# Performance work log

Measured on AMD Instinct MI355X. Metric: run time of the kernel, lower is better.

## Reference

```python
import jax, jax.numpy as jnp
import numpy as np

B, Q, K = 16, 8192, 8192
D_QK, D_V = 64, 64      # raw query/key and value feature dims
H = 8                    # num_heads
DP = 128                 # proj_qks output dim (per default MLP [128, 128])
VP = 64                  # proj_vs output dim (per default MLP [128, 64])
LN_EPS = 1e-6            # flax LayerNorm default


def setup_inputs() -> dict:
    key = jax.random.key(0)
    ks_ = jax.random.split(key, 12)
    f = lambda k, s: jax.random.normal(k, s, jnp.float32)
    return {
        "qs": f(ks_[0], (B, Q, D_QK)),
        "ks": f(ks_[1], (B, K, D_QK)),
        "vs": f(ks_[2], (B, K, D_V)),
        "qs_s": f(ks_[3], (B, Q, D_QK)),
        "ks_s": f(ks_[4], (B, K, D_QK)),
        "valid_lens": jax.random.randint(ks_[5], (B,), 1, K + 1, jnp.int32),
        # proj_qks = MLP([128, 128], gelu): Dense(128) -> gelu -> Dense(128)
        "Wq1": f(ks_[6], (2 * D_QK, DP)) / np.sqrt(2 * D_QK).astype(np.float32),
        "bq1": jnp.zeros((DP,), jnp.float32),
        "Wq2": f(ks_[7], (DP, DP)) / np.sqrt(DP).astype(np.float32),
        "bq2": jnp.zeros((DP,), jnp.float32),
        # proj_vs = MLP([128, 64], gelu): Dense(128) -> gelu -> Dense(64)
        "Wv1": f(ks_[8], (D_V, DP)) / np.sqrt(D_V).astype(np.float32),
        "bv1": jnp.zeros((DP,), jnp.float32),
        "Wv2": f(ks_[9], (DP, VP)) / np.sqrt(DP).astype(np.float32),
        "bv2": jnp.zeros((VP,), jnp.float32),
        "ln_scale": jnp.ones((VP,), jnp.float32),
        "ln_bias": jnp.zeros((VP,), jnp.float32),
    }


def _mlp2(x, W1, b1, W2, b2):
    # Dense -> gelu (tanh approx, flax default) -> Dense
    return jax.nn.gelu(x @ W1 + b1) @ W2 + b2


def reference(qs, ks, vs, qs_s, ks_s, valid_lens,
              Wq1, bq1, Wq2, bq2, Wv1, bv1, Wv2, bv2,
              ln_scale, ln_bias):
    Kl, D = ks.shape[-2], ks.shape[-1]  # D taken BEFORE stacking, as in source
    scale = D ** 0.25
    # stack spatial features then feature-map MLPs
    q = _mlp2(jnp.concatenate([qs_s, qs], axis=-1), Wq1, bq1, Wq2, bq2) / scale
    k = _mlp2(jnp.concatenate([ks_s, ks], axis=-1), Wq1, bq1, Wq2, bq2) / scale
    v = _mlp2(vs, Wv1, bv1, Wv2, bv2)
    # valid-length masking of keys, mean-style normalization of values
    mask = (jnp.arange(Kl)[None, :] < valid_lens[:, None]).astype(k.dtype)[..., None]
    k = k * mask
    v = v / valid_lens[:, None, None].astype(v.dtype)
    Bn, Qn = q.shape[0], q.shape[1]
    q = q.reshape(Bn, Qn, H, DP // H)   # B Q H d
    k = k.reshape(Bn, Kl, H, DP // H)   # B K H d
    v = v.reshape(Bn, Kl, H, VP // H)   # B K H e
    # linear attention: KV outer-product summary then apply queries
    kv = jnp.einsum('bkhd,bkhe->bhde', k, v)          # B H d e
    ctx = jnp.einsum('bqhd,bhde->bqhe', q, kv)        # B Q H e
    ctx = ctx.reshape(Bn, Qn, VP)
    # LayerNorm over last dim
    mu = ctx.mean(-1, keepdims=True)
    var = ((ctx - mu) ** 2).mean(-1, keepdims=True)
    return (ctx - mu) * jax.lax.rsqrt(var + LN_EPS) * ln_scale + ln_bias
```

## Files before the change

### kernel.cpp

```cpp
#include <hip/hip_runtime.h>
#include <hip/hip_bf16.h>


typedef __attribute__((ext_vector_type(8))) short short8;
typedef __attribute__((ext_vector_type(4))) float f32x4;
typedef unsigned int u32;
typedef unsigned short u16;

#define MFMA(A,B,C) __builtin_amdgcn_mfma_f32_16x16x32_bf16((A),(B),(C),0,0,0)
#define SBAR() __builtin_amdgcn_sched_barrier(0)

#define LDH 136
#define LDT 40
#define INVS 0.3535533905932738f

__device__ __forceinline__ u16 bfc(float x){
  __hip_bfloat16 h = __float2bfloat16(x);
  return __bfloat16_as_ushort(h);
}
__device__ __forceinline__ u32 pack2(float a, float b){
  return (u32)bfc(a) | ((u32)bfc(b) << 16);
}
__device__ __forceinline__ float b2f(u16 w){
  return __uint_as_float(((u32)w) << 16);
}
__device__ __forceinline__ short8 cvt8(f32x4 lo, f32x4 hi){
  short8 r;
  r[0]=(short)bfc(lo[0]); r[1]=(short)bfc(lo[1]);
  r[2]=(short)bfc(lo[2]); r[3]=(short)bfc(lo[3]);
  r[4]=(short)bfc(hi[0]); r[5]=(short)bfc(hi[1]);
  r[6]=(short)bfc(hi[2]); r[7]=(short)bfc(hi[3]);
  return r;
}
__device__ __forceinline__ float gelu_f(float x){
  float s = x*x;
  float u = x * __builtin_fmaf(s, 0.035677408136300125f, 0.7978845608028654f);
  float e = __builtin_amdgcn_exp2f(u * -2.885390081777927f);
  return x * __builtin_amdgcn_rcpf(1.0f + e);
}

__global__ void dk_prep(const float* __restrict__ Wq1, const float* __restrict__ Wq2,
                        const float* __restrict__ Wv1, const float* __restrict__ Wv2,
                        u16* __restrict__ wt){
  int i = blockIdx.x*256 + threadIdx.x;
  int e = i & 7;
  int lane = (i >> 3) & 63;
  int chunk = i >> 9;
  int c = lane & 15, g = lane >> 4;
  int k0 = 8*g + e;
  float v;
  if (chunk < 32){
    int mt = chunk >> 2, ks4 = chunk & 3;
    v = Wq1[(ks4*32 + k0)*128 + mt*16 + c];
  } else if (chunk < 64){
    int ch = chunk - 32; int mt = ch >> 2, ks4 = ch & 3;
    v = Wq2[(ks4*32 + k0)*128 + mt*16 + c] * INVS;
  } else if (chunk < 80){
    int ch = chunk - 64; int mt = ch >> 1, ks2 = ch & 1;
    v = Wv1[(ks2*32 + k0)*128 + mt*16 + c];
  } else {
    int ch = chunk - 80; int n2 = ch >> 2, ks4 = ch & 3;
    v = Wv2[(ks4*32 + k0)*64 + n2*16 + c];
  }
  wt[i] = bfc(v);
}

__global__ __launch_bounds__(128, 2) void dk_stage1(
    const float* __restrict__ ksp, const float* __restrict__ kssp,
    const float* __restrict__ vsp, const int* __restrict__ vlen,
    const float* __restrict__ bq1, const float* __restrict__ bq2,
    const float* __restrict__ bv1, const float* __restrict__ bv2,
    const u16* __restrict__ wt, float* __restrict__ kvgr, int repmask)
{
  __shared__ u16 sA[2][5120];
  __shared__ u16 sB[2][2560];
  const int tid = threadIdx.x;
  const int w = tid >> 6, l = tid & 63;
  const int c = l & 15, g = l >> 4;

  int pfx = (l < 16) ? ((vlen[l] + 63) >> 6) : 0;
  #pragma unroll
  for (int m=1; m<16; m<<=1){
    int v = __shfl_up(pfx, m, 64);
    if (l >= m) pfx += v;
  }
  const int T = __shfl(pfx, 15, 64);
  const int t = blockIdx.x;
  if (t >= T) return;
  unsigned long long mk = __ballot(l < 16 && pfx <= t);
  const int b = __popcll(mk);
  const int jb = t - (b ? __shfl(pfx, b-1, 64) : 0);
  const int len = vlen[b];
  const int rbase = jb*64 + w*32;
  if (rbase >= len) return;
  const int rep = t & repmask;
  const size_t row0 = (size_t)b*8192 + rbase;

  u16* H1 = sA[w];
  u16* KT = sA[w];
  u16* VT = sB[w];
  const u16* Wq1t = wt;
  const u16* Wq2t = wt + 16384;
  const u16* Wv1t = wt + 32768;
  const u16* Wv2t = wt + 40960;
  const f32x4 z4 = {0.f,0.f,0.f,0.f};

  {
    f32x4 xvf[8];
    #pragma unroll
    for (int ks2=0; ks2<2; ++ks2){
      #pragma unroll
      for (int nt=0; nt<2; ++nt){
        const float* src = vsp + (row0 + nt*16 + c)*64 + ks2*32 + 8*g;
        xvf[(ks2*2+nt)*2+0] = *(const f32x4*)src;
        xvf[(ks2*2+nt)*2+1] = *(const f32x4*)(src+4);
      }
    }
    SBAR();
    short8 xv[2][2];
    #pragma unroll
    for (int ks2=0; ks2<2; ++ks2)
      #pragma unroll
      for (int nt=0; nt<2; ++nt)
        xv[ks2][nt] = cvt8(xvf[(ks2*2+nt)*2+0], xvf[(ks2*2+nt)*2+1]);
    f32x4 av[8][2];
    #pragma unroll
    for (int mt=0; mt<8; ++mt){ av[mt][0]=z4; av[mt][1]=z4; }
    #pragma unroll
    for (int ks2=0; ks2<2; ++ks2){
      short8 wa[8];
      #pragma unroll
      for (int mt=0; mt<8; ++mt)
        wa[mt] = *(const short8*)&Wv1t[((mt*2+ks2)*64 + l)*8];
      SBAR();
      #pragma unroll
      for (int mt=0; mt<8; ++mt){
        av[mt][0] = MFMA(wa[mt], xv[ks2][0], av[mt][0]);
        av[mt][1] = MFMA(wa[mt], xv[ks2][1], av[mt][1]);
      }
    }
    #pragma unroll
    for (int mt=0; mt<8; ++mt){
      const f32x4 bia = *(const f32x4*)&bv1[mt*16 + 4*g];
      #pragma unroll
      for (int nt=0; nt<2; ++nt){
        uint2 pp;
        pp.x = pack2(gelu_f(av[mt][nt][0]+bia[0]), gelu_f(av[mt][nt][1]+bia[1]));
        pp.y = pack2(gelu_f(av[mt][nt][2]+bia[2]), gelu_f(av[mt][nt][3]+bia[3]));
        *(uint2*)&H1[(nt*16 + c)*LDH + mt*16 + 4*g] = pp;
      }
    }
  }
  {
    f32x4 acv[2][4];
    #pragma unroll
    for (int n2=0; n2<4; ++n2){ acv[0][n2]=z4; acv[1][n2]=z4; }
    #pragma unroll
    for (int ks4=0; ks4<4; ++ks4){
      short8 wb[4];
      #pragma unroll
      for (int n2=0; n2<4; ++n2)
        wb[n2] = *(const short8*)&Wv2t[((n2*4+ks4)*64 + l)*8];
      SBAR();
      const short8 ah0 = *(const short8*)&H1[(c     )*LDH + ks4*32 + 8*g];
      const short8 ah1 = *(const short8*)&H1[(16 + c)*LDH + ks4*32 + 8*g];
      #pragma unroll
      for (int n2=0; n2<4; ++n2){
        acv[0][n2] = MFMA(ah0, wb[n2], acv[0][n2]);
        acv[1][n2] = MFMA(ah1, wb[n2], acv[1][n2]);
      }
    }
    #pragma unroll
    for (int n2=0; n2<4; ++n2){
      const float bb = bv2[n2*16 + c];
      #pragma unroll
      for (int mt=0; mt<2; ++mt){
        uint2 pp;
        pp.x = pack2(acv[mt][n2][0]+bb, acv[mt][n2][1]+bb);
        pp.y = pack2(acv[mt][n2][2]+bb, acv[mt][n2][3]+bb);
        *(uint2*)&VT[(n2*16+c)*LDT + mt*16 + 4*g] = pp;
      }
    }
  }
  {
    f32x4 xkf[16];
    #pragma unroll
    for (int ks4=0; ks4<4; ++ks4){
      #pragma unroll
      for (int nt=0; nt<2; ++nt){
        const int kk = ks4*32 + 8*g;
        const float* src = (ks4 < 2) ? (kssp + (row0 + nt*16 + c)*64 + kk)
                                     : (ksp  + (row0 + nt*16 + c)*64 + (kk - 64));
        xkf[(ks4*2+nt)*2+0] = *(const f32x4*)src;
        xkf[(ks4*2+nt)*2+1] = *(const f32x4*)(src+4);
      }
    }
    SBAR();
    short8 xk[4][2];
    #pragma unroll
    for (int ks4=0; ks4<4; ++ks4)
      #pragma unroll
      for (int nt=0; nt<2; ++nt)
        xk[ks4][nt] = cvt8(xkf[(ks4*2+nt)*2+0], xkf[(ks4*2+nt)*2+1]);
    f32x4 acc[8][2];
    #pragma unroll
    for (int mt=0; mt<8; ++mt){ acc[mt][0]=z4; acc[mt][1]=z4; }
    #pragma unroll
    for (int ks4=0; ks4<4; ++ks4){
      short8 wa[8];
      #pragma unroll
      for (int mt=0; mt<8; ++mt)
        wa[mt] = *(const short8*)&Wq1t[((mt*4+ks4)*64 + l)*8];
      SBAR();
      #pragma unroll
      for (int mt=0; mt<8; ++mt){
        acc[mt][0] = MFMA(wa[mt], xk[ks4][0], acc[mt][0]);
        acc[mt][1] = MFMA(wa[mt], xk[ks4][1], acc[mt][1]);
      }
    }
    #pragma unroll
    for (int mt=0; mt<8; ++mt){
      const f32x4 bia = *(const f32x4*)&bq1[mt*16 + 4*g];
      #pragma unroll
      for (int nt=0; nt<2; ++nt){
        uint2 pp;
        pp.x = pack2(gelu_f(acc[mt][nt][0]+bia[0]), gelu_f(acc[mt][nt][1]+bia[1]));
        pp.y = pack2(gelu_f(acc[mt][nt][2]+bia[2]), gelu_f(acc[mt][nt][3]+bia[3]));
        *(uint2*)&H1[(nt*16 + c)*LDH + mt*16 + 4*g] = pp;
      }
    }
  }
  {
    f32x4 acc2[2][8];
    #pragma unroll
    for (int n2=0; n2<8; ++n2){ acc2[0][n2]=z4; acc2[1][n2]=z4; }
    #pragma unroll
    for (int ks4=0; ks4<4; ++ks4){
      short8 wb[8];
      #pragma unroll
      for (int n2=0; n2<8; ++n2)
        wb[n2] = *(const short8*)&Wq2t[((n2*4+ks4)*64 + l)*8];
      SBAR();
      const short8 ah0 = *(const short8*)&H1[(c     )*LDH + ks4*32 + 8*g];
      const short8 ah1 = *(const short8*)&H1[(16 + c)*LDH + ks4*32 + 8*g];
      #pragma unroll
      for (int n2=0; n2<8; ++n2){
        acc2[0][n2] = MFMA(ah0, wb[n2], acc2[0][n2]);
        acc2[1][n2] = MFMA(ah1, wb[n2], acc2[1][n2]);
      }
    }
    #pragma unroll
    for (int n2=0; n2<8; ++n2){
      const float bb = bq2[n2*16 + c] * INVS;
      #pragma unroll
      for (int mt=0; mt<2; ++mt){
        const int r0 = rbase + mt*16 + 4*g;
        float v0 = (r0+0 < len) ? acc2[mt][n2][0] + bb : 0.f;
        float v1 = (r0+1 < len) ? acc2[mt][n2][1] + bb : 0.f;
        float v2 = (r0+2 < len) ? acc2[mt][n2][2] + bb : 0.f;
        float v3 = (r0+3 < len) ? acc2[mt][n2][3] + bb : 0.f;
        uint2 pp; pp.x = pack2(v0,v1); pp.y = pack2(v2,v3);
        *(uint2*)&KT[(n2*16 + c)*LDT + mt*16 + 4*g] = pp;
      }
    }
  }
  {
    short8 zf = {0,0,0,0,0,0,0,0};
    f32x4 kvacc[8];
    #pragma unroll
    for (int h=0; h<8; ++h) kvacc[h] = z4;
    #pragma unroll
    for (int h=0; h<8; ++h){
      const short8 ka = *(const short8*)&KT[(h*16 + c)*LDT + 8*g];
      short8 vb = zf;
      if (c < 8) vb = *(const short8*)&VT[(h*8 + c)*LDT + 8*g];
      kvacc[h] = MFMA(ka, vb, kvacc[h]);
    }
    if (c < 8){
      float* kvg = kvgr + ((size_t)rep*16 + b)*1024;
      #pragma unroll
      for (int h=0; h<8; ++h){
        #pragma unroll
        for (int r=0; r<4; ++r)
          atomicAdd(&kvg[(h*16 + 4*g + r)*8 + c], kvacc[h][r]);
      }
    }
  }
}

__global__ void dk_mid(const float* __restrict__ kvgr, int nrep,
                       const int* __restrict__ vlen,
                       const float* __restrict__ bq2,
                       const u16* __restrict__ wt,
                       u16* __restrict__ Mt, float* __restrict__ c0g)
{
  __shared__ float kvs[1024];
  const int b = blockIdx.x, t = threadIdx.x;
  const float inv_len = 1.0f / (float)vlen[b];
  #pragma unroll
  for (int k=0; k<4; ++k){
    const int idx = t + 256*k;
    float s = 0.f;
    for (int r=0; r<nrep; ++r) s += kvgr[((size_t)r*16 + b)*1024 + idx];
    kvs[idx] = s * inv_len;
  }
  __syncthreads();
  for (int k=0; k<32; ++k){
    const int o = t + 256*k;
    const int e = o >> 7, j = o & 127;
    const int h = e >> 3, e8 = e & 7;
    const int ks4 = j >> 5, gg = (j >> 3) & 3, el = j & 7;
    float s = 0.f;
    #pragma unroll
    for (int d=0; d<16; ++d){
      const int od = h*16 + d;
      const u16 wv = wt[16384 + (((od>>4)*4 + ks4)*64 + gg*16 + (od&15))*8 + el];
      s += b2f(wv) * kvs[h*128 + d*8 + e8];
    }
    const int n3 = e >> 4, cc = e & 15;
    Mt[(size_t)b*8192 + ((n3*4 + ks4)*64 + gg*16 + cc)*8 + el] = bfc(s);
  }
  if (t < 64){
    const int e = t, h = e >> 3, e8 = e & 7;
    float s = 0.f;
    #pragma unroll
    for (int d=0; d<16; ++d)
      s += bq2[h*16+d] * INVS * kvs[h*128 + d*8 + e8];
    c0g[b*64 + e] = s;
  }
}

__global__ __launch_bounds__(128, 2) void dk_stage2(
    const float* __restrict__ qsp, const float* __restrict__ qssp,
    const float* __restrict__ bq1,
    const float* __restrict__ lnw_g, const float* __restrict__ lnb_g,
    const u16* __restrict__ wt, const u16* __restrict__ Mt,
    const float* __restrict__ c0g, float* __restrict__ outp)
{
  __shared__ u16 sH1[2][32*LDH];
  const int tid = threadIdx.x;
  const int w = tid >> 6, l = tid & 63;
  const int c = l & 15, g = l >> 4;
  const int b  = blockIdx.x >> 7;
  const int jb = blockIdx.x & 127;
  const int rbase = jb*64 + w*32;
  u16* H1 = sH1[w];
  const u16* Wq1t = wt;
  const size_t row0 = (size_t)b*8192 + rbase;
  const f32x4 z4 = {0.f,0.f,0.f,0.f};

  {
    f32x4 xqf[16];
    #pragma unroll
    for (int ks4=0; ks4<4; ++ks4){
      #pragma unroll
      for (int nt=0; nt<2; ++nt){
        const int kk = ks4*32 + 8*g;
        const float* src = (ks4 < 2) ? (qssp + (row0 + nt*16 + c)*64 + kk)
                                     : (qsp  + (row0 + nt*16 + c)*64 + (kk - 64));
        xqf[(ks4*2+nt)*2+0] = *(const f32x4*)src;
        xqf[(ks4*2+nt)*2+1] = *(const f32x4*)(src+4);
      }
    }
    SBAR();
    short8 xq[4][2];
    #pragma unroll
    for (int ks4=0; ks4<4; ++ks4)
      #pragma unroll
      for (int nt=0; nt<2; ++nt)
        xq[ks4][nt] = cvt8(xqf[(ks4*2+nt)*2+0], xqf[(ks4*2+nt)*2+1]);
    f32x4 acc[8][2];
    #pragma unroll
    for (int mt=0; mt<8; ++mt){ acc[mt][0]=z4; acc[mt][1]=z4; }
    #pragma unroll
    for (int ks4=0; ks4<4; ++ks4){
      short8 wa[8];
      #pragma unroll
      for (int mt=0; mt<8; ++mt)
        wa[mt] = *(const short8*)&Wq1t[((mt*4+ks4)*64 + l)*8];
      SBAR();
      #pragma unroll
      for (int mt=0; mt<8; ++mt){
        acc[mt][0] = MFMA(wa[mt], xq[ks4][0], acc[mt][0]);
        acc[mt][1] = MFMA(wa[mt], xq[ks4][1], acc[mt][1]);
      }
    }
    #pragma unroll
    for (int mt=0; mt<8; ++mt){
      const f32x4 bia = *(const f32x4*)&bq1[mt*16 + 4*g];
      #pragma unroll
      for (int nt=0; nt<2; ++nt){
        uint2 pp;
        pp.x = pack2(gelu_f(acc[mt][nt][0]+bia[0]), gelu_f(acc[mt][nt][1]+bia[1]));
        pp.y = pack2(gelu_f(acc[mt][nt][2]+bia[2]), gelu_f(acc[mt][nt][3]+bia[3]));
        *(uint2*)&H1[(nt*16 + c)*LDH + mt*16 + 4*g] = pp;
      }
    }
  }
  f32x4 acc3[2][4];
  #pragma unroll
  for (int n3=0; n3<4; ++n3){ acc3[0][n3]=z4; acc3[1][n3]=z4; }
  const u16* Mb = Mt + (size_t)b*8192;
  {
    short8 bm[16];
    #pragma unroll
    for (int ks4=0; ks4<4; ++ks4)
      #pragma unroll
      for (int n3=0; n3<4; ++n3)
        bm[ks4*4+n3] = *(const short8*)&Mb[((n3*4+ks4)*64 + l)*8];
    SBAR();
    #pragma unroll
    for (int ks4=0; ks4<4; ++ks4){
      const short8 aq0 = *(const short8*)&H1[(c     )*LDH + ks4*32 + 8*g];
      const short8 aq1 = *(const short8*)&H1[(16 + c)*LDH + ks4*32 + 8*g];
      #pragma unroll
      for (int n3=0; n3<4; ++n3){
        acc3[0][n3] = MFMA(aq0, bm[ks4*4+n3], acc3[0][n3]);
        acc3[1][n3] = MFMA(aq1, bm[ks4*4+n3], acc3[1][n3]);
      }
    }
  }
  float c0v[4];
  #pragma unroll
  for (int n3=0; n3<4; ++n3) c0v[n3] = c0g[b*64 + n3*16 + c];
  float lnw[4], lnb[4];
  #pragma unroll
  for (int n3=0; n3<4; ++n3){ lnw[n3] = lnw_g[n3*16 + c]; lnb[n3] = lnb_g[n3*16 + c]; }
  float* Tb = (float*)H1;
  #pragma unroll
  for (int mt=0; mt<2; ++mt){
    #pragma unroll
    for (int r=0; r<4; ++r){
      float s1 = 0.f, s2 = 0.f;
      #pragma unroll
      for (int n3=0; n3<4; ++n3){
        float v = acc3[mt][n3][r] + c0v[n3];
        s1 += v; s2 += v*v;
      }
      #pragma unroll
      for (int m=1; m<16; m<<=1){
        s1 += __shfl_xor(s1, m, 64);
        s2 += __shfl_xor(s2, m, 64);
      }
      const float mu = s1 * (1.0f/64.0f);
      const float var = s2 * (1.0f/64.0f) - mu*mu;
      const float rs = rsqrtf(var + 1e-6f);
      const int rloc = mt*16 + 4*g + r;
      #pragma unroll
      for (int n3=0; n3<4; ++n3)
        Tb[rloc*68 + n3*16 + c] = (acc3[mt][n3][r] + c0v[n3] - mu)*rs*lnw[n3] + lnb[n3];
    }
  }
  float* ob = outp + row0*64;
  #pragma unroll
  for (int i=0; i<8; ++i){
    const int row = i*4 + (l>>4);
    const f32x4 vv = *(const f32x4*)&Tb[row*68 + (l&15)*4];
    *(f32x4*)(ob + row*64 + (l&15)*4) = vv;
  }
}

extern "C" void kernel_launch(void* const* d_in, const int* in_sizes, int n_in,
                              void* d_out, int out_size, void* d_ws, size_t ws_size,
                              hipStream_t stream)
{
  const float* qs   = (const float*)d_in[0];
  const float* ks   = (const float*)d_in[1];
  const float* vs   = (const float*)d_in[2];
  const float* qs_s = (const float*)d_in[3];
  const float* ks_s = (const float*)d_in[4];
  const int*   vl   = (const int*)d_in[5];
  const float* Wq1  = (const float*)d_in[6];
  const float* bq1  = (const float*)d_in[7];
  const float* Wq2  = (const float*)d_in[8];
  const float* bq2  = (const float*)d_in[9];
  const float* Wv1  = (const float*)d_in[10];
  const float* bv1  = (const float*)d_in[11];
  const float* Wv2  = (const float*)d_in[12];
  const float* bv2  = (const float*)d_in[13];
  const float* lnw  = (const float*)d_in[14];
  const float* lnb  = (const float*)d_in[15];
  (void)in_sizes; (void)n_in; (void)out_size;

  const size_t fixed = 96*1024 + 256*1024 + 4096;
  int nrep = 4;
  while (nrep > 1 && (size_t)nrep*65536 + fixed > ws_size) nrep >>= 1;
  float* kvgr = (float*)d_ws;
  u16*   wt   = (u16*)((char*)d_ws + (size_t)nrep*65536);
  u16*   Mt   = (u16*)((char*)wt + 96*1024);
  float* c0   = (float*)((char*)Mt + 256*1024);

  hipMemsetAsync(kvgr, 0, (size_t)nrep*65536, stream);
  dk_prep<<<192, 256, 0, stream>>>(Wq1, Wq2, Wv1, Wv2, wt);
  dk_stage1<<<2048, 128, 0, stream>>>(ks, ks_s, vs, vl, bq1, bq2, bv1, bv2,
                                      wt, kvgr, nrep - 1);
  dk_mid<<<16, 256, 0, stream>>>(kvgr, nrep, vl, bq2, wt, Mt, c0);
  dk_stage2<<<2048, 128, 0, stream>>>(qs, qs_s, bq1, lnw, lnb, wt, Mt, c0,
                                      (float*)d_out);
}
```

Before: 92.17 us.

## Stage weights in LDS via direct global-to-LDS loads with persistent grid-stride blocks

Both stage kernels now copy the pre-swizzled bf16 weight tiles into shared memory once per block using global_load_lds. The kernels then become persistent, grid-stride loops over tiles, with smaller grids (256 and 768 blocks), so each weight copy is reused across many tiles. This replaces repeated per-tile weight fetches from global/L2 with LDS reads. In exchange, stage1 uses about 96KB of LDS per block, which caps occupancy at one or few blocks per CU. There are also fewer waves to hide memory latency.

```diff
diff --git a/kernel.cpp b/kernel.cpp
--- a/kernel.cpp
+++ b/kernel.cpp
@@ -37,6 +37,11 @@
   float u = x * __builtin_fmaf(s, 0.035677408136300125f, 0.7978845608028654f);
   float e = __builtin_amdgcn_exp2f(u * -2.885390081777927f);
   return x * __builtin_amdgcn_rcpf(1.0f + e);
+}
+__device__ __forceinline__ void gld_lds16(const u16* gsrc, u16* ldst){
+  __builtin_amdgcn_global_load_lds(
+      (const __attribute__((address_space(1))) void*)gsrc,
+      (__attribute__((address_space(3))) void*)ldst, 16, 0, 0);
 }
 
 __global__ void dk_prep(const float* __restrict__ Wq1, const float* __restrict__ Wq2,
@@ -65,7 +70,7 @@
   wt[i] = bfc(v);
 }
 
-__global__ __launch_bounds__(128, 2) void dk_stage1(
+__global__ __launch_bounds__(128, 1) void dk_stage1(
     const float* __restrict__ ksp, const float* __restrict__ kssp,
     const float* __restrict__ vsp, const int* __restrict__ vlen,
     const float* __restrict__ bq1, const float* __restrict__ bq2,
@@ -74,9 +79,16 @@
 {
   __shared__ u16 sA[2][5120];
   __shared__ u16 sB[2][2560];
+  __shared__ u16 sW[49152];
   const int tid = threadIdx.x;
   const int w = tid >> 6, l = tid & 63;
   const int c = l & 15, g = l >> 4;
+
+  #pragma unroll
+  for (int j=0; j<48; ++j){
+    const int ch = w*48 + j;
+    gld_lds16(wt + ((size_t)ch*64 + l)*8, &sW[(size_t)ch*512]);
+  }
 
   int pfx = (l < 16) ? ((vlen[l] + 63) >> 6) : 0;
   #pragma unroll
@@ -85,204 +97,202 @@
     if (l >= m) pfx += v;
   }
   const int T = __shfl(pfx, 15, 64);
-  const int t = blockIdx.x;
-  if (t >= T) return;
-  unsigned long long mk = __ballot(l < 16 && pfx <= t);
-  const int b = __popcll(mk);
-  const int jb = t - (b ? __shfl(pfx, b-1, 64) : 0);
-  const int len = vlen[b];
-  const int rbase = jb*64 + w*32;
-  if (rbase >= len) return;
-  const int rep = t & repmask;
-  const size_t row0 = (size_t)b*8192 + rbase;
+  __syncthreads();
 
   u16* H1 = sA[w];
   u16* KT = sA[w];
   u16* VT = sB[w];
-  const u16* Wq1t = wt;
-  const u16* Wq2t = wt + 16384;
-  const u16* Wv1t = wt + 32768;
-  const u16* Wv2t = wt + 40960;
   const f32x4 z4 = {0.f,0.f,0.f,0.f};
 
-  {
-    f32x4 xvf[8];
-    #pragma unroll
-    for (int ks2=0; ks2<2; ++ks2){
-      #pragma unroll
-      for (int nt=0; nt<2; ++nt){
-        const float* src = vsp + (row0 + nt*16 + c)*64 + ks2*32 + 8*g;
-        xvf[(ks2*2+nt)*2+0] = *(const f32x4*)src;
-        xvf[(ks2*2+nt)*2+1] = *(const f32x4*)(src+4);
-      }
-    }
-    SBAR();
-    short8 xv[2][2];
-    #pragma unroll
-    for (int ks2=0; ks2<2; ++ks2)
-      #pragma unroll
-      for (int nt=0; nt<2; ++nt)
-        xv[ks2][nt] = cvt8(xvf[(ks2*2+nt)*2+0], xvf[(ks2*2+nt)*2+1]);
-    f32x4 av[8][2];
-    #pragma unroll
-    for (int mt=0; mt<8; ++mt){ av[mt][0]=z4; av[mt][1]=z4; }
-    #pragma unroll
-    for (int ks2=0; ks2<2; ++ks2){
-      short8 wa[8];
-      #pragma unroll
-      for (int mt=0; mt<8; ++mt)
-        wa[mt] = *(const short8*)&Wv1t[((mt*2+ks2)*64 + l)*8];
+  for (int t = blockIdx.x; t < T; t += gridDim.x){
+    unsigned long long mk = __ballot(l < 16 && pfx <= t);
+    const int b = __popcll(mk);
+    const int jb = t - (b ? __shfl(pfx, b-1, 64) : 0);
+    const int len = vlen[b];
+    const int rbase = jb*64 + w*32;
+    if (rbase >= len) continue;
+    const int rep = t & repmask;
+    const size_t row0 = (size_t)b*8192 + rbase;
+
+    {
+      f32x4 xvf[8];
+      #pragma unroll
+      for (int ks2=0; ks2<2; ++ks2){
+        #pragma unroll
+        for (int nt=0; nt<2; ++nt){
+          const float* src = vsp + (row0 + nt*16 + c)*64 + ks2*32 + 8*g;
+          xvf[(ks2*2+nt)*2+0] = *(const f32x4*)src;
+          xvf[(ks2*2+nt)*2+1] = *(const f32x4*)(src+4);
+        }
+      }
       SBAR();
+      short8 xv[2][2];
+      #pragma unroll
+      for (int ks2=0; ks2<2; ++ks2)
+        #pragma unroll
+        for (int nt=0; nt<2; ++nt)
+          xv[ks2][nt] = cvt8(xvf[(ks2*2+nt)*2+0], xvf[(ks2*2+nt)*2+1]);
+      f32x4 av[8][2];
+      #pragma unroll
+      for (int mt=0; mt<8; ++mt){ av[mt][0]=z4; av[mt][1]=z4; }
+      #pragma unroll
+      for (int ks2=0; ks2<2; ++ks2){
+        short8 wa[8];
+        #pragma unroll
+        for (int mt=0; mt<8; ++mt)
+          wa[mt] = *(const short8*)&sW[(size_t)(64 + mt*2+ks2)*512 + l*8];
+        SBAR();
+        #pragma unroll
+        for (int mt=0; mt<8; ++mt){
+          av[mt][0] = MFMA(wa[mt], xv[ks2][0], av[mt][0]);
+          av[mt][1] = MFMA(wa[mt], xv[ks2][1], av[mt][1]);
+        }
+      }
       #pragma unroll
       for (int mt=0; mt<8; ++mt){
-        av[mt][0] = MFMA(wa[mt], xv[ks2][0], av[mt][0]);
-        av[mt][1] = MFMA(wa[mt], xv[ks2][1], av[mt][1]);
-      }
-    }
-    #pragma unroll
-    for (int mt=0; mt<8; ++mt){
-      const f32x4 bia = *(const f32x4*)&bv1[mt*16 + 4*g];
-      #pragma unroll
-      for (int nt=0; nt<2; ++nt){
-        uint2 pp;
-        pp.x = pack2(gelu_f(av[mt][nt][0]+bia[0]), gelu_f(av[mt][nt][1]+bia[1]));
-        pp.y = pack2(gelu_f(av[mt][nt][2]+bia[2]), gelu_f(av[mt][nt][3]+bia[3]));
-        *(uint2*)&H1[(nt*16 + c)*LDH + mt*16 + 4*g] = pp;
-      }
-    }
-  }
-  {
-    f32x4 acv[2][4];
-    #pragma unroll
-    for (int n2=0; n2<4; ++n2){ acv[0][n2]=z4; acv[1][n2]=z4; }
-    #pragma unroll
-    for (int ks4=0; ks4<4; ++ks4){
-      short8 wb[4];
-      #pragma unroll
-      for (int n2=0; n2<4; ++n2)
-        wb[n2] = *(const short8*)&Wv2t[((n2*4+ks4)*64 + l)*8];
+        const f32x4 bia = *(const f32x4*)&bv1[mt*16 + 4*g];
+        #pragma unroll
+        for (int nt=0; nt<2; ++nt){
+          uint2 pp;
+          pp.x = pack2(gelu_f(av[mt][nt][0]+bia[0]), gelu_f(av[mt][nt][1]+bia[1]));
+          pp.y = pack2(gelu_f(av[mt][nt][2]+bia[2]), gelu_f(av[mt][nt][3]+bia[3]));
+          *(uint2*)&H1[(nt*16 + c)*LDH + mt*16 + 4*g] = pp;
+        }
+      }
+    }
+    {
+      f32x4 acv[2][4];
+      #pragma unroll
+      for (int n2=0; n2<4; ++n2){ acv[0][n2]=z4; acv[1][n2]=z4; }
+      #pragma unroll
+      for (int ks4=0; ks4<4; ++ks4){
+        short8 wb[4];
+        #pragma unroll
+        for (int n2=0; n2<4; ++n2)
+          wb[n2] = *(const short8*)&sW[(size_t)(80 + n2*4+ks4)*512 + l*8];
+        SBAR();
+        const short8 ah0 = *(const short8*)&H1[(c     )*LDH + ks4*32 + 8*g];
+        const short8 ah1 = *(const short8*)&H1[(16 + c)*LDH + ks4*32 + 8*g];
+        #pragma unroll
+        for (int n2=0; n2<4; ++n2){
+          acv[0][n2] = MFMA(ah0, wb[n2], acv[0][n2]);
+          acv[1][n2] = MFMA(ah1, wb[n2], acv[1][n2]);
+        }
+      }
+      #pragma unroll
+      for (int n2=0; n2<4; ++n2){
+        const float bb = bv2[n2*16 + c];
+        #pragma unroll
+        for (int mt=0; mt<2; ++mt){
+          uint2 pp;
+          pp.x = pack2(acv[mt][n2][0]+bb, acv[mt][n2][1]+bb);
+          pp.y = pack2(acv[mt][n2][2]+bb, acv[mt][n2][3]+bb);
+          *(uint2*)&VT[(n2*16+c)*LDT + mt*16 + 4*g] = pp;
+        }
+      }
+    }
+    {
+      f32x4 xkf[16];
+      #pragma unroll
+      for (int ks4=0; ks4<4; ++ks4){
+        #pragma unroll
+        for (int nt=0; nt<2; ++nt){
+          const int kk = ks4*32 + 8*g;
+          const float* src = (ks4 < 2) ? (kssp + (row0 + nt*16 + c)*64 + kk)
+                                       : (ksp  + (row0 + nt*16 + c)*64 + (kk - 64));
+          xkf[(ks4*2+nt)*2+0] = *(const f32x4*)src;
+          xkf[(ks4*2+nt)*2+1] = *(const f32x4*)(src+4);
+        }
+      }
       SBAR();
-      const short8 ah0 = *(const short8*)&H1[(c     )*LDH + ks4*32 + 8*g];
-      const short8 ah1 = *(const short8*)&H1[(16 + c)*LDH + ks4*32 + 8*g];
-      #pragma unroll
-      for (int n2=0; n2<4; ++n2){
-        acv[0][n2] = MFMA(ah0, wb[n2], acv[0][n2]);
-        acv[1][n2] = MFMA(ah1, wb[n2], acv[1][n2]);
-      }
-    }
-    #pragma unroll
-    for (int n2=0; n2<4; ++n2){
-      const float bb = bv2[n2*16 + c];
-      #pragma unroll
-      for (int mt=0; mt<2; ++mt){
-        uint2 pp;
-        pp.x = pack2(acv[mt][n2][0]+bb, acv[mt][n2][1]+bb);
-        pp.y = pack2(acv[mt][n2][2]+bb, acv[mt][n2][3]+bb);
-        *(uint2*)&VT[(n2*16+c)*LDT + mt*16 + 4*g] = pp;
-      }
-    }
-  }
-  {
-    f32x4 xkf[16];
-    #pragma unroll
-    for (int ks4=0; ks4<4; ++ks4){
-      #pragma unroll
-      for (int nt=0; nt<2; ++nt){
-        const int kk = ks4*32 + 8*g;
-        const float* src = (ks4 < 2) ? (kssp + (row0 + nt*16 + c)*64 + kk)
-                                     : (ksp  + (row0 + nt*16 + c)*64 + (kk - 64));
-        xkf[(ks4*2+nt)*2+0] = *(const f32x4*)src;
-        xkf[(ks4*2+nt)*2+1] = *(const f32x4*)(src+4);
-      }
-    }
-    SBAR();
-    short8 xk[4][2];
-    #pragma unroll
-    for (int ks4=0; ks4<4; ++ks4)
-      #pragma unroll
-      for (int nt=0; nt<2; ++nt)
-        xk[ks4][nt] = cvt8(xkf[(ks4*2+nt)*2+0], xkf[(ks4*2+nt)*2+1]);
-    f32x4 acc[8][2];
-    #pragma unroll
-    for (int mt=0; mt<8; ++mt){ acc[mt][0]=z4; acc[mt][1]=z4; }
-    #pragma unroll
-    for (int ks4=0; ks4<4; ++ks4){
-      short8 wa[8];
-      #pragma unroll
-      for (int mt=0; mt<8; ++mt)
-        wa[mt] = *(const short8*)&Wq1t[((mt*4+ks4)*64 + l)*8];
-      SBAR();
+      short8 xk[4][2];
+      #pragma unroll
+      for (int ks4=0; ks4<4; ++ks4)
+        #pragma unroll
+        for (int nt=0; nt<2; ++nt)
+          xk[ks4][nt] = cvt8(xkf[(ks4*2+nt)*2+0], xkf[(ks4*2+nt)*2+1]);
+      f32x4 acc[8][2];
+      #pragma unroll
+      for (int mt=0; mt<8; ++mt){ acc[mt][0]=z4; acc[mt][1]=z4; }
+      #pragma unroll
+      for (int ks4=0; ks4<4; ++ks4){
+        short8 wa[8];
+        #pragma unroll
+        for (int mt=0; mt<8; ++mt)
+          wa[mt] = *(const short8*)&sW[(size_t)(mt*4+ks4)*512 + l*8];
+        SBAR();
+        #pragma unroll
+        for (int mt=0; mt<8; ++mt){
+          acc[mt][0] = MFMA(wa[mt], xk[ks4][0], acc[mt][0]);
+          acc[mt][1] = MFMA(wa[mt], xk[ks4][1], acc[mt][1]);
+        }
+      }
       #pragma unroll
       for (int mt=0; mt<8; ++mt){
-        acc[mt][0] = MFMA(wa[mt], xk[ks4][0], acc[mt][0]);
-        acc[mt][1] = MFMA(wa[mt], xk[ks4][1], acc[mt][1]);
-      }
-    }
-    #pragma unroll
-    for (int mt=0; mt<8; ++mt){
-      const f32x4 bia = *(const f32x4*)&bq1[mt*16 + 4*g];
-      #pragma unroll
-      for (int nt=0; nt<2; ++nt){
-        uint2 pp;
-        pp.x = pack2(gelu_f(acc[mt][nt][0]+bia[0]), gelu_f(acc[mt][nt][1]+bia[1]));
-        pp.y = pack2(gelu_f(acc[mt][nt][2]+bia[2]), gelu_f(acc[mt][nt][3]+bia[3]));
-        *(uint2*)&H1[(nt*16 + c)*LDH + mt*16 + 4*g] = pp;
-      }
-    }
-  }
-  {
-    f32x4 acc2[2][8];
-    #pragma unroll
-    for (int n2=0; n2<8; ++n2){ acc2[0][n2]=z4; acc2[1][n2]=z4; }
-    #pragma unroll
-    for (int ks4=0; ks4<4; ++ks4){
-      short8 wb[8];
-      #pragma unroll
-      for (int n2=0; n2<8; ++n2)
-        wb[n2] = *(const short8*)&Wq2t[((n2*4+ks4)*64 + l)*8];
-      SBAR();
-      const short8 ah0 = *(const short8*)&H1[(c     )*LDH + ks4*32 + 8*g];
-      const short8 ah1 = *(const short8*)&H1[(16 + c)*LDH + ks4*32 + 8*g];
+        const f32x4 bia = *(const f32x4*)&bq1[mt*16 + 4*g];
+        #pragma unroll
+        for (int nt=0; nt<2; ++nt){
+          uint2 pp;
+          pp.x = pack2(gelu_f(acc[mt][nt][0]+bia[0]), gelu_f(acc[mt][nt][1]+bia[1]));
+          pp.y = pack2(gelu_f(acc[mt][nt][2]+bia[2]), gelu_f(acc[mt][nt][3]+bia[3]));
+          *(uint2*)&H1[(nt*16 + c)*LDH + mt*16 + 4*g] = pp;
+        }
+      }
+    }
+    {
+      f32x4 acc2[2][8];
+      #pragma unroll
+      for (int n2=0; n2<8; ++n2){ acc2[0][n2]=z4; acc2[1][n2]=z4; }
+      #pragma unroll
+      for (int ks4=0; ks4<4; ++ks4){
+        short8 wb[8];
+        #pragma unroll
+        for (int n2=0; n2<8; ++n2)
+          wb[n2] = *(const short8*)&sW[(size_t)(32 + n2*4+ks4)*512 + l*8];
+        SBAR();
+        const short8 ah0 = *(const short8*)&H1[(c     )*LDH + ks4*32 + 8*g];
+        const short8 ah1 = *(const short8*)&H1[(16 + c)*LDH + ks4*32 + 8*g];
+        #pragma unroll
+        for (int n2=0; n2<8; ++n2){
+          acc2[0][n2] = MFMA(ah0, wb[n2], acc2[0][n2]);
+          acc2[1][n2] = MFMA(ah1, wb[n2], acc2[1][n2]);
+        }
+      }
       #pragma unroll
       for (int n2=0; n2<8; ++n2){
-        acc2[0][n2] = MFMA(ah0, wb[n2], acc2[0][n2]);
-        acc2[1][n2] = MFMA(ah1, wb[n2], acc2[1][n2]);
-      }
-    }
-    #pragma unroll
-    for (int n2=0; n2<8; ++n2){
-      const float bb = bq2[n2*16 + c] * INVS;
-      #pragma unroll
-      for (int mt=0; mt<2; ++mt){
-        const int r0 = rbase + mt*16 + 4*g;
-        float v0 = (r0+0 < len) ? acc2[mt][n2][0] + bb : 0.f;
-        float v1 = (r0+1 < len) ? acc2[mt][n2][1] + bb : 0.f;
-        float v2 = (r0+2 < len) ? acc2[mt][n2][2] + bb : 0.f;
-        float v3 = (r0+3 < len) ? acc2[mt][n2][3] + bb : 0.f;
-        uint2 pp; pp.x = pack2(v0,v1); pp.y = pack2(v2,v3);
-        *(uint2*)&KT[(n2*16 + c)*LDT + mt*16 + 4*g] = pp;
-      }
-    }
-  }
-  {
-    short8 zf = {0,0,0,0,0,0,0,0};
-    f32x4 kvacc[8];
-    #pragma unroll
-    for (int h=0; h<8; ++h) kvacc[h] = z4;
-    #pragma unroll
-    for (int h=0; h<8; ++h){
-      const short8 ka = *(const short8*)&KT[(h*16 + c)*LDT + 8*g];
-      short8 vb = zf;
-      if (c < 8) vb = *(const short8*)&VT[(h*8 + c)*LDT + 8*g];
-      kvacc[h] = MFMA(ka, vb, kvacc[h]);
-    }
-    if (c < 8){
-      float* kvg = kvgr + ((size_t)rep*16 + b)*1024;
+        const float bb = bq2[n2*16 + c] * INVS;
+        #pragma unroll
+        for (int mt=0; mt<2; ++mt){
+          const int r0 = rbase + mt*16 + 4*g;
+          float v0 = (r0+0 < len) ? acc2[mt][n2][0] + bb : 0.f;
+          float v1 = (r0+1 < len) ? acc2[mt][n2][1] + bb : 0.f;
+          float v2 = (r0+2 < len) ? acc2[mt][n2][2] + bb : 0.f;
+          float v3 = (r0+3 < len) ? acc2[mt][n2][3] + bb : 0.f;
+          uint2 pp; pp.x = pack2(v0,v1); pp.y = pack2(v2,v3);
+          *(uint2*)&KT[(n2*16 + c)*LDT + mt*16 + 4*g] = pp;
+        }
+      }
+    }
+    {
+      short8 zf = {0,0,0,0,0,0,0,0};
+      f32x4 kvacc[8];
+      #pragma unroll
+      for (int h=0; h<8; ++h) kvacc[h] = z4;
       #pragma unroll
       for (int h=0; h<8; ++h){
-        #pragma unroll
-        for (int r=0; r<4; ++r)
-          atomicAdd(&kvg[(h*16 + 4*g + r)*8 + c], kvacc[h][r]);
+        const short8 ka = *(const short8*)&KT[(h*16 + c)*LDT + 8*g];
+        short8 vb = zf;
+        if (c < 8) vb = *(const short8*)&VT[(h*8 + c)*LDT + 8*g];
+        kvacc[h] = MFMA(ka, vb, kvacc[h]);
+      }
+      if (c < 8){
+        float* kvg = kvgr + ((size_t)rep*16 + b)*1024;
+        #pragma unroll
+        for (int h=0; h<8; ++h){
+          #pragma unroll
+          for (int r=0; r<4; ++r)
+            atomicAdd(&kvg[(h*16 + 4*g + r)*8 + c], kvacc[h][r]);
+        }
       }
     }
   }
@@ -330,7 +340,7 @@
   }
 }
 
-__global__ __launch_bounds__(128, 2) void dk_stage2(
+__global__ __launch_bounds__(128, 1) void dk_stage2(
     const float* __restrict__ qsp, const float* __restrict__ qssp,
     const float* __restrict__ bq1,
     const float* __restrict__ lnw_g, const float* __restrict__ lnb_g,
@@ -338,125 +348,135 @@
     const float* __restrict__ c0g, float* __restrict__ outp)
 {
   __shared__ u16 sH1[2][32*LDH];
+  __shared__ u16 sW[16384];
   const int tid = threadIdx.x;
   const int w = tid >> 6, l = tid & 63;
   const int c = l & 15, g = l >> 4;
-  const int b  = blockIdx.x >> 7;
-  const int jb = blockIdx.x & 127;
-  const int rbase = jb*64 + w*32;
   u16* H1 = sH1[w];
-  const u16* Wq1t = wt;
-  const size_t row0 = (size_t)b*8192 + rbase;
   const f32x4 z4 = {0.f,0.f,0.f,0.f};
 
-  {
-    f32x4 xqf[16];
-    #pragma unroll
-    for (int ks4=0; ks4<4; ++ks4){
-      #pragma unroll
-      for (int nt=0; nt<2; ++nt){
-        const int kk = ks4*32 + 8*g;
-        const float* src = (ks4 < 2) ? (qssp + (row0 + nt*16 + c)*64 + kk)
-                                     : (qsp  + (row0 + nt*16 + c)*64 + (kk - 64));
-        xqf[(ks4*2+nt)*2+0] = *(const f32x4*)src;
-        xqf[(ks4*2+nt)*2+1] = *(const f32x4*)(src+4);
-      }
-    }
-    SBAR();
-    short8 xq[4][2];
-    #pragma unroll
-    for (int ks4=0; ks4<4; ++ks4)
-      #pragma unroll
-      for (int nt=0; nt<2; ++nt)
-        xq[ks4][nt] = cvt8(xqf[(ks4*2+nt)*2+0], xqf[(ks4*2+nt)*2+1]);
-    f32x4 acc[8][2];
-    #pragma unroll
-    for (int mt=0; mt<8; ++mt){ acc[mt][0]=z4; acc[mt][1]=z4; }
-    #pragma unroll
-    for (int ks4=0; ks4<4; ++ks4){
-      short8 wa[8];
-      #pragma unroll
-      for (int mt=0; mt<8; ++mt)
-        wa[mt] = *(const short8*)&Wq1t[((mt*4+ks4)*64 + l)*8];
+  #pragma unroll
+  for (int j=0; j<16; ++j){
+    const int ch = w*16 + j;
+    gld_lds16(wt + ((size_t)ch*64 + l)*8, &sW[(size_t)ch*512]);
+  }
+  __syncthreads();
+
+  for (int t = blockIdx.x; t < 2048; t += gridDim.x){
+    const int b  = t >> 7;
+    const int jb = t & 127;
+    const int rbase = jb*64 + w*32;
+    const size_t row0 = (size_t)b*8192 + rbase;
+    const u16* Mb = Mt + (size_t)b*8192;
+
+    {
+      f32x4 xqf[16];
+      #pragma unroll
+      for (int ks4=0; ks4<4; ++ks4){
+        #pragma unroll
+        for (int nt=0; nt<2; ++nt){
+          const int kk = ks4*32 + 8*g;
+          const float* src = (ks4 < 2) ? (qssp + (row0 + nt*16 + c)*64 + kk)
+                                       : (qsp  + (row0 + nt*16 + c)*64 + (kk - 64));
+          xqf[(ks4*2+nt)*2+0] = *(const f32x4*)src;
+          xqf[(ks4*2+nt)*2+1] = *(const f32x4*)(src+4);
+        }
+      }
       SBAR();
+      short8 xq[4][2];
+      #pragma unroll
+      for (int ks4=0; ks4<4; ++ks4)
+        #pragma unroll
+        for (int nt=0; nt<2; ++nt)
+          xq[ks4][nt] = cvt8(xqf[(ks4*2+nt)*2+0], xqf[(ks4*2+nt)*2+1]);
+      f32x4 acc[8][2];
+      #pragma unroll
+      for (int mt=0; mt<8; ++mt){ acc[mt][0]=z4; acc[mt][1]=z4; }
+      #pragma unroll
+      for (int ks4=0; ks4<4; ++ks4){
+        short8 wa[8];
+        #pragma unroll
+        for (int mt=0; mt<8; ++mt)
+          wa[mt] = *(const short8*)&sW[(size_t)(mt*4+ks4)*512 + l*8];
+        SBAR();
+        #pragma unroll
+        for (int mt=0; mt<8; ++mt){
+          acc[mt][0] = MFMA(wa[mt], xq[ks4][0], acc[mt][0]);
+          acc[mt][1] = MFMA(wa[mt], xq[ks4][1], acc[mt][1]);
+        }
+      }
       #pragma unroll
       for (int mt=0; mt<8; ++mt){
-        acc[mt][0] = MFMA(wa[mt], xq[ks4][0], acc[mt][0]);
-        acc[mt][1] = MFMA(wa[mt], xq[ks4][1], acc[mt][1]);
-      }
-    }
-    #pragma unroll
-    for (int mt=0; mt<8; ++mt){
-      const f32x4 bia = *(const f32x4*)&bq1[mt*16 + 4*g];
-      #pragma unroll
-      for (int nt=0; nt<2; ++nt){
-        uint2 pp;
-        pp.x = pack2(gelu_f(acc[mt][nt][0]+bia[0]), gelu_f(acc[mt][nt][1]+bia[1]));
-        pp.y = pack2(gelu_f(acc[mt][nt][2]+bia[2]), gelu_f(acc[mt][nt][3]+bia[3]));
-        *(uint2*)&H1[(nt*16 + c)*LDH + mt*16 + 4*g] = pp;
-      }
-    }
-  }
-  f32x4 acc3[2][4];
-  #pragma unroll
-  for (int n3=0; n3<4; ++n3){ acc3[0][n3]=z4; acc3[1][n3]=z4; }
-  const u16* Mb = Mt + (size_t)b*8192;
-  {
-    short8 bm[16];
-    #pragma unroll
-    for (int ks4=0; ks4<4; ++ks4)
-      #pragma unroll
-      for (int n3=0; n3<4; ++n3)
-        bm[ks4*4+n3] = *(const short8*)&Mb[((n3*4+ks4)*64 + l)*8];
-    SBAR();
-    #pragma unroll
-    for (int ks4=0; ks4<4; ++ks4){
-      const short8 aq0 = *(const short8*)&H1[(c     )*LDH + ks4*32 + 8*g];
-      const short8 aq1 = *(const short8*)&H1[(16 + c)*LDH + ks4*32 + 8*g];
-      #pragma unroll
-      for (int n3=0; n3<4; ++n3){
-        acc3[0][n3] = MFMA(aq0, bm[ks4*4+n3], acc3[0][n3]);
-        acc3[1][n3] = MFMA(aq1, bm[ks4*4+n3], acc3[1][n3]);
-      }
-    }
-  }
-  float c0v[4];
-  #pragma unroll
-  for (int n3=0; n3<4; ++n3) c0v[n3] = c0g[b*64 + n3*16 + c];
-  float lnw[4], lnb[4];
-  #pragma unroll
-  for (int n3=0; n3<4; ++n3){ lnw[n3] = lnw_g[n3*16 + c]; lnb[n3] = lnb_g[n3*16 + c]; }
-  float* Tb = (float*)H1;
-  #pragma unroll
-  for (int mt=0; mt<2; ++mt){
-    #pragma unroll
-    for (int r=0; r<4; ++r){
-      float s1 = 0.f, s2 = 0.f;
-      #pragma unroll
-      for (int n3=0; n3<4; ++n3){
-        float v = acc3[mt][n3][r] + c0v[n3];
-        s1 += v; s2 += v*v;
-      }
-      #pragma unroll
-      for (int m=1; m<16; m<<=1){
-        s1 += __shfl_xor(s1, m, 64);
-        s2 += __shfl_xor(s2, m, 64);
-      }
-      const float mu = s1 * (1.0f/64.0f);
-      const float var = s2 * (1.0f/64.0f) - mu*mu;
-      const float rs = rsqrtf(var + 1e-6f);
-      const int rloc = mt*16 + 4*g + r;
-      #pragma unroll
-      for (int n3=0; n3<4; ++n3)
-        Tb[rloc*68 + n3*16 + c] = (acc3[mt][n3][r] + c0v[n3] - mu)*rs*lnw[n3] + lnb[n3];
-    }
-  }
-  float* ob = outp + row0*64;
-  #pragma unroll
-  for (int i=0; i<8; ++i){
-    const int row = i*4 + (l>>4);
-    const f32x4 vv = *(const f32x4*)&Tb[row*68 + (l&15)*4];
-    *(f32x4*)(ob + row*64 + (l&15)*4) = vv;
+        const f32x4 bia = *(const f32x4*)&bq1[mt*16 + 4*g];
+        #pragma unroll
+        for (int nt=0; nt<2; ++nt){
+          uint2 pp;
+          pp.x = pack2(gelu_f(acc[mt][nt][0]+bia[0]), gelu_f(acc[mt][nt][1]+bia[1]));
+          pp.y = pack2(gelu_f(acc[mt][nt][2]+bia[2]), gelu_f(acc[mt][nt][3]+bia[3]));
+          *(uint2*)&H1[(nt*16 + c)*LDH + mt*16 + 4*g] = pp;
+        }
+      }
+    }
+    f32x4 acc3[2][4];
+    #pragma unroll
+    for (int n3=0; n3<4; ++n3){ acc3[0][n3]=z4; acc3[1][n3]=z4; }
+    {
+      short8 bm[16];
+      #pragma unroll
+      for (int ks4=0; ks4<4; ++ks4)
+        #pragma unroll
+        for (int n3=0; n3<4; ++n3)
+          bm[ks4*4+n3] = *(const short8*)&Mb[((n3*4+ks4)*64 + l)*8];
+      SBAR();
+      #pragma unroll
+      for (int ks4=0; ks4<4; ++ks4){
+        const short8 aq0 = *(const short8*)&H1[(c     )*LDH + ks4*32 + 8*g];
+        const short8 aq1 = *(const short8*)&H1[(16 + c)*LDH + ks4*32 + 8*g];
+        #pragma unroll
+        for (int n3=0; n3<4; ++n3){
+          acc3[0][n3] = MFMA(aq0, bm[ks4*4+n3], acc3[0][n3]);
+          acc3[1][n3] = MFMA(aq1, bm[ks4*4+n3], acc3[1][n3]);
+        }
+      }
+    }
+    float c0v[4];
+    #pragma unroll
+    for (int n3=0; n3<4; ++n3) c0v[n3] = c0g[b*64 + n3*16 + c];
+    float lnw[4], lnb[4];
+    #pragma unroll
+    for (int n3=0; n3<4; ++n3){ lnw[n3] = lnw_g[n3*16 + c]; lnb[n3] = lnb_g[n3*16 + c]; }
+    float* Tb = (float*)H1;
+    #pragma unroll
+    for (int mt=0; mt<2; ++mt){
+      #pragma unroll
+      for (int r=0; r<4; ++r){
+        float s1 = 0.f, s2 = 0.f;
+        #pragma unroll
+        for (int n3=0; n3<4; ++n3){
+          float v = acc3[mt][n3][r] + c0v[n3];
+          s1 += v; s2 += v*v;
+        }
+        #pragma unroll
+        for (int m=1; m<16; m<<=1){
+          s1 += __shfl_xor(s1, m, 64);
+          s2 += __shfl_xor(s2, m, 64);
+        }
+        const float mu = s1 * (1.0f/64.0f);
+        const float var = s2 * (1.0f/64.0f) - mu*mu;
+        const float rs = rsqrtf(var + 1e-6f);
+        const int rloc = mt*16 + 4*g + r;
+        #pragma unroll
+        for (int n3=0; n3<4; ++n3)
+          Tb[rloc*68 + n3*16 + c] = (acc3[mt][n3][r] + c0v[n3] - mu)*rs*lnw[n3] + lnb[n3];
+      }
+    }
+    float* ob = outp + row0*64;
+    #pragma unroll
+    for (int i=0; i<8; ++i){
+      const int row = i*4 + (l>>4);
+      const f32x4 vv = *(const f32x4*)&Tb[row*68 + (l&15)*4];
+      *(f32x4*)(ob + row*64 + (l&15)*4) = vv;
+    }
   }
 }
 
@@ -492,9 +512,9 @@
 
   hipMemsetAsync(kvgr, 0, (size_t)nrep*65536, stream);
   dk_prep<<<192, 256, 0, stream>>>(Wq1, Wq2, Wv1, Wv2, wt);
-  dk_stage1<<<2048, 128, 0, stream>>>(ks, ks_s, vs, vl, bq1, bq2, bv1, bv2,
-                                      wt, kvgr, nrep - 1);
+  dk_stage1<<<256, 128, 0, stream>>>(ks, ks_s, vs, vl, bq1, bq2, bv1, bv2,
+                                     wt, kvgr, nrep - 1);
   dk_mid<<<16, 256, 0, stream>>>(kvgr, nrep, vl, bq2, wt, Mt, c0);
-  dk_stage2<<<2048, 128, 0, stream>>>(qs, qs_s, bq1, lnw, lnb, wt, Mt, c0,
-                                      (float*)d_out);
-}
+  dk_stage2<<<768, 128, 0, stream>>>(qs, qs_s, bq1, lnw, lnb, wt, Mt, c0,
+                                     (float*)d_out);
+}
```

Measured after the change: 111.7 us. +21.2%, slower.
